# Kernel tuning notes

Measured on AMD Instinct MI355X. Metric: run time of the kernel, lower is better.

## Reference

```python
import jax, jax.numpy as jnp
import numpy as np

N = 50000
E = 800000
F_IN, F_HID, F_OUT = 128, 128, 64


def setup_inputs() -> dict:
    key = jax.random.key(0)
    ks = jax.random.split(key, 8)
    x = jax.random.normal(ks[0], (N, F_IN), dtype=jnp.float32)
    attn_edge_index = jax.random.randint(ks[1], (2, E), 0, N, dtype=jnp.int64)
    attn_edge_weight = jax.random.uniform(ks[2], (E,), dtype=jnp.float32)
    # GCNConv params (glorot-ish scale); PyG lin has no bias, conv bias added after aggregation
    W1 = jax.random.normal(ks[3], (F_IN, F_HID), dtype=jnp.float32) * (1.0 / np.sqrt(F_IN))
    b1 = jnp.zeros((F_HID,), dtype=jnp.float32)
    W2 = jax.random.normal(ks[4], (F_HID, F_OUT), dtype=jnp.float32) * (1.0 / np.sqrt(F_HID))
    b2 = jnp.zeros((F_OUT,), dtype=jnp.float32)
    return {"x": x, "attn_edge_index": attn_edge_index, "attn_edge_weight": attn_edge_weight,
            "W1": W1, "b1": b1, "W2": W2, "b2": b2}


def _gcn_norm(edge_index, edge_weight, num_nodes):
    # Add self-loops with weight 1 (PyG gcn_norm default)
    loop = jnp.arange(num_nodes, dtype=edge_index.dtype)
    src = jnp.concatenate([edge_index[0], loop])
    dst = jnp.concatenate([edge_index[1], loop])
    w = jnp.concatenate([edge_weight, jnp.ones((num_nodes,), edge_weight.dtype)])
    deg = jax.ops.segment_sum(w, dst, num_segments=num_nodes)  # in-degree weighted
    dinv = jnp.where(deg > 0, jax.lax.rsqrt(deg), 0.0)
    norm = dinv[src] * w * dinv[dst]  # symmetric normalization
    return src, dst, norm


def _gcn_conv(h, src, dst, norm, W, b, num_nodes):
    h = h @ W                                   # [N, Fout] dense transform
    msg = norm[:, None] * h[src]                # [E+N, Fout] gather-multiply
    out = jax.ops.segment_sum(msg, dst, num_segments=num_nodes)  # scatter-add
    return out + b


def reference(x, attn_edge_index, attn_edge_weight, W1, b1, W2, b2):
    num_nodes = x.shape[0]
    src, dst, norm = _gcn_norm(attn_edge_index, attn_edge_weight, num_nodes)
    h = _gcn_conv(x, src, dst, norm, W1, b1, num_nodes)
    h = jax.nn.relu(h)
    # dropout(p=0.5) is identity in eval mode
    h = _gcn_conv(h, src, dst, norm, W2, b2, num_nodes)
    return h
```

## Files before the change

### kernel.cpp

```cpp
#include <hip/hip_runtime.h>
#include <hip/hip_bf16.h>

static constexpr int FIN   = 128;
static constexpr int FHID  = 128;
static constexpr int FOUTC = 64;
static constexpr int CAP   = 64;

typedef short bf16x8 __attribute__((ext_vector_type(8)));
typedef float f32x4 __attribute__((ext_vector_type(4)));
typedef unsigned u32x4 __attribute__((ext_vector_type(4)));

__device__ __forceinline__ float bfbits2f(unsigned short u) {
  union { unsigned i; float f; } c; c.i = ((unsigned)u) << 16; return c.f;
}
__device__ __forceinline__ void unpack_bf2(unsigned u, float& lo, float& hi) {
  union { unsigned i; float f; } a, b;
  a.i = u << 16;
  b.i = u & 0xffff0000u;
  lo = a.f; hi = b.f;
}
__device__ __forceinline__ unsigned short f2bfbits(float f) {
  union { float fv; unsigned i; } c; c.fv = f;
  unsigned i = c.i;
  unsigned r = i + 0x7FFFu + ((i >> 16) & 1u);
  if ((i & 0x7F800000u) == 0x7F800000u) r = i;
  return (unsigned short)(r >> 16);
}
__device__ __forceinline__ int ld_idx(const void* ei, int is64, long long off) {
  return is64 ? (int)((const long long*)ei)[off] : ((const int*)ei)[off];
}
__device__ __forceinline__ float ld_f(const void* p, int isbf, long long i) {
  return isbf ? bfbits2f(((const unsigned short*)p)[i]) : ((const float*)p)[i];
}

__global__ void setup_kernel(const unsigned short* __restrict__ xb,
                             const unsigned* __restrict__ eiw,
                             const void* __restrict__ W1, const void* __restrict__ W2,
                             int* __restrict__ flags, unsigned short* __restrict__ Wt1,
                             unsigned short* __restrict__ Wt2, uint4* __restrict__ zr,
                             int nz4, int nztot) {
  const int tid = threadIdx.x;
  const int gid = blockIdx.x * 256 + tid;
  __shared__ int sflags[2];
  if (tid < 64) {
    unsigned short xs = xb[2 * tid];
    unsigned long long mb = __ballot(((xs >> 7) & 0xFFu) >= 0xC0u);
    unsigned long long m2 = __ballot(eiw[2 * tid + 1] != 0u);
    if (tid == 0) {
      sflags[0] = (mb == 0ull);
      sflags[1] = (m2 == 0ull);
      if (blockIdx.x == 0) { flags[0] = sflags[0]; flags[1] = sflags[1]; }
    }
  }
  __syncthreads();
  int f = sflags[0];
  if (blockIdx.x < 96) {
    int i = gid;
    if (i < 128 * 128) {
      int k = i >> 7, nn = i & 127;
      Wt1[nn * 128 + k] = f2bfbits(ld_f(W1, f, i));
    } else {
      int j = i - 128 * 128;
      int k = j >> 6, nn = j & 63;
      Wt2[nn * 128 + k] = f2bfbits(ld_f(W2, f, j));
    }
  }
  uint4 z = make_uint4(0u, 0u, 0u, 0u);
  for (int j = gid; j < nz4; j += gridDim.x * 256) zr[j] = z;
  if (gid == 0) {
    for (int j = nz4 * 4; j < nztot; ++j) ((unsigned*)zr)[j] = 0u;
  }
}

__global__ void fill_edges(const void* __restrict__ ei, const void* __restrict__ ew,
                           const int* __restrict__ flg, unsigned* __restrict__ cnt,
                           float* __restrict__ deg, unsigned* __restrict__ cedge, int E) {
  int g = blockIdx.x * 256 + threadIdx.x;
  if (g >= E) return;
  int is64 = flg[1], isbf = flg[0];
  int s = ld_idx(ei, is64, g);
  int d = ld_idx(ei, is64, (long long)E + g);
  float w = ld_f(ew, isbf, g);
  unsigned pos = atomicAdd(&cnt[d], 1u);
  atomicAdd(&deg[d], w);
  if (pos < (unsigned)CAP)
    cedge[(size_t)d * CAP + pos] = (((unsigned)s) << 16) | (unsigned)f2bfbits(w);
}

__launch_bounds__(256)
__global__ void gather_l1(const void* __restrict__ x, const int* __restrict__ flg,
                          const unsigned* __restrict__ cedge, const unsigned* __restrict__ cnt,
                          const float* __restrict__ deg, unsigned* __restrict__ agg, int n) {
  int wid = (blockIdx.x * 256 + threadIdx.x) >> 6;
  int lane = threadIdx.x & 63;
  if (wid >= n) return;
  unsigned e = __builtin_nontemporal_load(cedge + (size_t)wid * CAP + lane);
  int c = (int)cnt[wid];
  c = c > CAP ? CAP : c;
  float dw = deg[wid];
  float di = rsqrtf(1.f + dw);
  int rs = (lane < c) ? (int)(e >> 16) : wid;
  float ds = deg[rs];
  float wv = (lane < c) ? bfbits2f((unsigned short)(e & 0xFFFFu)) : 1.f;
  int cp = c + 1; if (cp > 64) cp = 64;
  float rw = (lane < cp) ? wv * rsqrtf(1.f + ds) : 0.f;
  int iters = (cp + 15) >> 4;

  if (flg[0]) {
    const uint4* xv = (const uint4*)x;
    const int fgrp = lane & 15, egrp = lane >> 4;
    float acc[8];
#pragma unroll
    for (int k = 0; k < 8; ++k) acc[k] = 0.f;

#define L1_LOAD(UA, UB, UC, UD, WA, WB, WC, WD, base)                       \
    {                                                                       \
      int i0 = (base) + egrp, i1 = i0 + 4, i2 = i0 + 8, i3 = i0 + 12;       \
      int s0 = __shfl(rs, i0), s1 = __shfl(rs, i1);                         \
      int s2 = __shfl(rs, i2), s3 = __shfl(rs, i3);                         \
      UA = xv[(size_t)s0 * 16 + fgrp];                                      \
      UB = xv[(size_t)s1 * 16 + fgrp];                                      \
      UC = xv[(size_t)s2 * 16 + fgrp];                                      \
      UD = xv[(size_t)s3 * 16 + fgrp];                                      \
      WA = __shfl(rw, i0); WB = __shfl(rw, i1);                             \
      WC = __shfl(rw, i2); WD = __shfl(rw, i3);                             \
    }
#define L1_FMA(U, W)                                                        \
    { float l, h;                                                           \
      unpack_bf2(U.x, l, h); acc[0]=fmaf(W,l,acc[0]); acc[1]=fmaf(W,h,acc[1]); \
      unpack_bf2(U.y, l, h); acc[2]=fmaf(W,l,acc[2]); acc[3]=fmaf(W,h,acc[3]); \
      unpack_bf2(U.z, l, h); acc[4]=fmaf(W,l,acc[4]); acc[5]=fmaf(W,h,acc[5]); \
      unpack_bf2(U.w, l, h); acc[6]=fmaf(W,l,acc[6]); acc[7]=fmaf(W,h,acc[7]); }
#define L1_FMA4(UA,UB,UC,UD,WA,WB,WC,WD) \
    L1_FMA(UA,WA) L1_FMA(UB,WB) L1_FMA(UC,WC) L1_FMA(UD,WD)

    uint4 a0, a1, a2, a3, b0, b1, b2, b3;
    float wa0, wa1, wa2, wa3, wb0, wb1, wb2, wb3;
    L1_LOAD(a0, a1, a2, a3, wa0, wa1, wa2, wa3, 0);
    if (iters > 1) {
      L1_LOAD(b0, b1, b2, b3, wb0, wb1, wb2, wb3, 16);
      L1_FMA4(a0, a1, a2, a3, wa0, wa1, wa2, wa3);
      if (iters > 2) {
        L1_LOAD(a0, a1, a2, a3, wa0, wa1, wa2, wa3, 32);
        L1_FMA4(b0, b1, b2, b3, wb0, wb1, wb2, wb3);
        if (iters > 3) {
          L1_LOAD(b0, b1, b2, b3, wb0, wb1, wb2, wb3, 48);
          L1_FMA4(a0, a1, a2, a3, wa0, wa1, wa2, wa3);
          L1_FMA4(b0, b1, b2, b3, wb0, wb1, wb2, wb3);
        } else {
          L1_FMA4(a0, a1, a2, a3, wa0, wa1, wa2, wa3);
        }
      } else {
        L1_FMA4(b0, b1, b2, b3, wb0, wb1, wb2, wb3);
      }
    } else {
      L1_FMA4(a0, a1, a2, a3, wa0, wa1, wa2, wa3);
    }
#undef L1_LOAD
#undef L1_FMA
#undef L1_FMA4

#pragma unroll
    for (int k = 0; k < 8; ++k) {
      acc[k] += __shfl_xor(acc[k], 16);
      acc[k] += __shfl_xor(acc[k], 32);
    }
    if (lane < 16) {
      float o0 = di * acc[0], o1 = di * acc[1], o2 = di * acc[2], o3 = di * acc[3];
      float o4 = di * acc[4], o5 = di * acc[5], o6 = di * acc[6], o7 = di * acc[7];
      u32x4 pk;
      pk.x = (unsigned)f2bfbits(o0) | ((unsigned)f2bfbits(o1) << 16);
      pk.y = (unsigned)f2bfbits(o2) | ((unsigned)f2bfbits(o3) << 16);
      pk.z = (unsigned)f2bfbits(o4) | ((unsigned)f2bfbits(o5) << 16);
      pk.w = (unsigned)f2bfbits(o6) | ((unsigned)f2bfbits(o7) << 16);
      __builtin_nontemporal_store(pk, (u32x4*)agg + (size_t)wid * 16 + fgrp);
    }
  } else {
    const float4* xf = (const float4*)x;
    const int fgrp = lane & 31, egrp = lane >> 5;
    float acc[4] = {0.f, 0.f, 0.f, 0.f};
    int it8 = (cp + 7) >> 3;
    for (int it = 0; it < it8; ++it) {
      int b = it * 8 + egrp;
#pragma unroll
      for (int t = 0; t < 4; ++t) {
        int idx = b + t * 2;
        int s = __shfl(rs, idx);
        float w = __shfl(rw, idx);
        float4 v = xf[(size_t)s * 32 + fgrp];
        acc[0] = fmaf(w, v.x, acc[0]); acc[1] = fmaf(w, v.y, acc[1]);
        acc[2] = fmaf(w, v.z, acc[2]); acc[3] = fmaf(w, v.w, acc[3]);
      }
    }
#pragma unroll
    for (int k = 0; k < 4; ++k) acc[k] += __shfl_xor(acc[k], 32);
    if (lane < 32) {
      float o0 = di * acc[0], o1 = di * acc[1], o2 = di * acc[2], o3 = di * acc[3];
      uint2 pk;
      pk.x = (unsigned)f2bfbits(o0) | ((unsigned)f2bfbits(o1) << 16);
      pk.y = (unsigned)f2bfbits(o2) | ((unsigned)f2bfbits(o3) << 16);
      ((uint2*)agg)[(size_t)wid * 32 + fgrp] = pk;
    }
  }
}

__launch_bounds__(256)
__global__ void gather_l2(const unsigned short* __restrict__ hw2, const int* __restrict__ flg,
                          const unsigned* __restrict__ cedge, const unsigned* __restrict__ cnt,
                          const float* __restrict__ deg, const void* __restrict__ b2,
                          void* __restrict__ out, int n) {
  int wid = (blockIdx.x * 256 + threadIdx.x) >> 6;
  int lane = threadIdx.x & 63;
  if (wid >= n) return;
  unsigned e = __builtin_nontemporal_load(cedge + (size_t)wid * CAP + lane);
  int c = (int)cnt[wid];
  c = c > CAP ? CAP : c;
  float dw = deg[wid];
  float di = rsqrtf(1.f + dw);
  int rs = (lane < c) ? (int)(e >> 16) : wid;
  float ds = deg[rs];
  float wv = (lane < c) ? bfbits2f((unsigned short)(e & 0xFFFFu)) : 1.f;
  int cp = c + 1; if (cp > 64) cp = 64;
  float rw = (lane < cp) ? wv * rsqrtf(1.f + ds) : 0.f;
  int iters = (cp + 15) >> 4;

  const uint4* hv = (const uint4*)hw2;
  const int fgrp = lane & 7, egrp = lane >> 3;
  float acc[8];
#pragma unroll
  for (int k = 0; k < 8; ++k) acc[k] = 0.f;

#define L2_LOAD(UA, UB, WA, WB, base)                                   \
  { int i0 = (base) + egrp, i1 = i0 + 8;                                \
    int s0 = __shfl(rs, i0), s1 = __shfl(rs, i1);                       \
    UA = hv[(size_t)s0 * 8 + fgrp];                                     \
    UB = hv[(size_t)s1 * 8 + fgrp];                                     \
    WA = __shfl(rw, i0); WB = __shfl(rw, i1); }
#define L2_FMA(U, W)                                                    \
  { float l, h;                                                         \
    unpack_bf2(U.x, l, h); acc[0]=fmaf(W,l,acc[0]); acc[1]=fmaf(W,h,acc[1]); \
    unpack_bf2(U.y, l, h); acc[2]=fmaf(W,l,acc[2]); acc[3]=fmaf(W,h,acc[3]); \
    unpack_bf2(U.z, l, h); acc[4]=fmaf(W,l,acc[4]); acc[5]=fmaf(W,h,acc[5]); \
    unpack_bf2(U.w, l, h); acc[6]=fmaf(W,l,acc[6]); acc[7]=fmaf(W,h,acc[7]); }
#define L2_FMA2(UA, UB, WA, WB) L2_FMA(UA, WA) L2_FMA(UB, WB)

  uint4 a0, a1, b0, b1;
  float wa0, wa1, wb0, wb1;
  L2_LOAD(a0, a1, wa0, wa1, 0);
  if (iters > 1) {
    L2_LOAD(b0, b1, wb0, wb1, 16);
    L2_FMA2(a0, a1, wa0, wa1);
    if (iters > 2) {
      L2_LOAD(a0, a1, wa0, wa1, 32);
      L2_FMA2(b0, b1, wb0, wb1);
      if (iters > 3) {
        L2_LOAD(b0, b1, wb0, wb1, 48);
        L2_FMA2(a0, a1, wa0, wa1);
        L2_FMA2(b0, b1, wb0, wb1);
      } else {
        L2_FMA2(a0, a1, wa0, wa1);
      }
    } else {
      L2_FMA2(b0, b1, wb0, wb1);
    }
  } else {
    L2_FMA2(a0, a1, wa0, wa1);
  }
#undef L2_LOAD
#undef L2_FMA
#undef L2_FMA2

#pragma unroll
  for (int k = 0; k < 8; ++k) {
    acc[k] += __shfl_xor(acc[k], 8);
    acc[k] += __shfl_xor(acc[k], 16);
    acc[k] += __shfl_xor(acc[k], 32);
  }
  if (lane < 8) {
    int isbf = flg[0];
    float o0 = di * acc[0] + ld_f(b2, isbf, fgrp * 8 + 0);
    float o1 = di * acc[1] + ld_f(b2, isbf, fgrp * 8 + 1);
    float o2 = di * acc[2] + ld_f(b2, isbf, fgrp * 8 + 2);
    float o3 = di * acc[3] + ld_f(b2, isbf, fgrp * 8 + 3);
    float o4 = di * acc[4] + ld_f(b2, isbf, fgrp * 8 + 4);
    float o5 = di * acc[5] + ld_f(b2, isbf, fgrp * 8 + 5);
    float o6 = di * acc[6] + ld_f(b2, isbf, fgrp * 8 + 6);
    float o7 = di * acc[7] + ld_f(b2, isbf, fgrp * 8 + 7);
    if (isbf) {
      uint4 pk;
      pk.x = (unsigned)f2bfbits(o0) | ((unsigned)f2bfbits(o1) << 16);
      pk.y = (unsigned)f2bfbits(o2) | ((unsigned)f2bfbits(o3) << 16);
      pk.z = (unsigned)f2bfbits(o4) | ((unsigned)f2bfbits(o5) << 16);
      pk.w = (unsigned)f2bfbits(o6) | ((unsigned)f2bfbits(o7) << 16);
      ((uint4*)out)[(size_t)wid * 8 + fgrp] = pk;
    } else {
      ((float4*)out)[(size_t)wid * 16 + fgrp * 2 + 0] = make_float4(o0, o1, o2, o3);
      ((float4*)out)[(size_t)wid * 16 + fgrp * 2 + 1] = make_float4(o4, o5, o6, o7);
    }
  }
}

__launch_bounds__(256)
__global__ void gemm12(const unsigned short* __restrict__ agg1,
                       const unsigned short* __restrict__ Wt1,
                       const unsigned short* __restrict__ Wt2,
                       const void* __restrict__ b1, const int* __restrict__ flg,
                       unsigned short* __restrict__ hw2, int M) {
  __shared__ unsigned short As[128 * 128];
  __shared__ unsigned short W1s[128 * 128];
  __shared__ unsigned short W2s[64 * 128];
  const int tid = threadIdx.x;
  const int r0 = blockIdx.x * 128;

  for (int i = tid; i < 128 * 16; i += 256) {
    int r = i >> 4, ch = i & 15;
    uint4 v = make_uint4(0u, 0u, 0u, 0u);
    if (r0 + r < M) v = *(const uint4*)(agg1 + (size_t)(r0 + r) * 128 + ch * 8);
    *(uint4*)&As[r * 128 + ((ch ^ (r & 15)) << 3)] = v;
  }
  for (int i = tid; i < 128 * 16; i += 256) {
    int r = i >> 4, ch = i & 15;
    uint4 v = *(const uint4*)(Wt1 + (size_t)r * 128 + ch * 8);
    *(uint4*)&W1s[r * 128 + ((ch ^ (r & 15)) << 3)] = v;
  }
  for (int i = tid; i < 64 * 16; i += 256) {
    int r = i >> 4, ch = i & 15;
    uint4 v = *(const uint4*)(Wt2 + (size_t)r * 128 + ch * 8);
    *(uint4*)&W2s[r * 128 + ((ch ^ (r & 15)) << 3)] = v;
  }
  __syncthreads();

  const int lane = tid & 63;
  const int wv = tid >> 6;
  const int ln15 = lane & 15;
  const int kq = lane >> 4;
  const int wbf = flg[0];

  f32x4 acc1[2][8];
#pragma unroll
  for (int mi = 0; mi < 2; ++mi)
#pragma unroll
    for (int nt = 0; nt < 8; ++nt) acc1[mi][nt] = (f32x4){0.f, 0.f, 0.f, 0.f};
#pragma unroll
  for (int kc = 0; kc < 4; ++kc) {
    int coff = (((kc * 4 + kq) ^ ln15) << 3);
    bf16x8 a0 = *(const bf16x8*)&As[((2 * wv + 0) * 16 + ln15) * 128 + coff];
    bf16x8 a1 = *(const bf16x8*)&As[((2 * wv + 1) * 16 + ln15) * 128 + coff];
#pragma unroll
    for (int nt = 0; nt < 8; ++nt) {
      bf16x8 b = *(const bf16x8*)&W1s[(nt * 16 + ln15) * 128 + coff];
      acc1[0][nt] = __builtin_amdgcn_mfma_f32_16x16x32_bf16(a0, b, acc1[0][nt], 0, 0, 0);
      acc1[1][nt] = __builtin_amdgcn_mfma_f32_16x16x32_bf16(a1, b, acc1[1][nt], 0, 0, 0);
    }
  }

#pragma unroll
  for (int nt = 0; nt < 8; ++nt) {
    int col = nt * 16 + ln15;
    float bv = ld_f(b1, wbf, col);
#pragma unroll
    for (int mi = 0; mi < 2; ++mi) {
#pragma unroll
      for (int r = 0; r < 4; ++r) {
        int row = 32 * wv + mi * 16 + kq * 4 + r;
        float o = fmaxf(acc1[mi][nt][r] + bv, 0.f);
        As[row * 128 + ((((col >> 3)) ^ (row & 15)) << 3) + (col & 7)] = f2bfbits(o);
      }
    }
  }
  __syncthreads();

  f32x4 acc2[2][4];
#pragma unroll
  for (int mi = 0; mi < 2; ++mi)
#pragma unroll
    for (int nt = 0; nt < 4; ++nt) acc2[mi][nt] = (f32x4){0.f, 0.f, 0.f, 0.f};
#pragma unroll
  for (int kc = 0; kc < 4; ++kc) {
    int coff = (((kc * 4 + kq) ^ ln15) << 3);
    bf16x8 a0 = *(const bf16x8*)&As[((2 * wv + 0) * 16 + ln15) * 128 + coff];
    bf16x8 a1 = *(const bf16x8*)&As[((2 * wv + 1) * 16 + ln15) * 128 + coff];
#pragma unroll
    for (int nt = 0; nt < 4; ++nt) {
      bf16x8 b = *(const bf16x8*)&W2s[(nt * 16 + ln15) * 128 + coff];
      acc2[0][nt] = __builtin_amdgcn_mfma_f32_16x16x32_bf16(a0, b, acc2[0][nt], 0, 0, 0);
      acc2[1][nt] = __builtin_amdgcn_mfma_f32_16x16x32_bf16(a1, b, acc2[1][nt], 0, 0, 0);
    }
  }
#pragma unroll
  for (int nt = 0; nt < 4; ++nt) {
    int col = nt * 16 + ln15;
#pragma unroll
    for (int mi = 0; mi < 2; ++mi) {
#pragma unroll
      for (int r = 0; r < 4; ++r) {
        int gr = r0 + 32 * wv + mi * 16 + kq * 4 + r;
        if (gr < M) hw2[(size_t)gr * 64 + col] = f2bfbits(acc2[mi][nt][r]);
      }
    }
  }
}

extern "C" void kernel_launch(void* const* d_in, const int* in_sizes, int n_in, void* d_out,
                              int out_size, void* d_ws, size_t ws_size, hipStream_t stream) {
  const void* x  = d_in[0];
  const void* ei = d_in[1];
  const void* ew = d_in[2];
  const void* W1 = d_in[3];
  const void* b1 = d_in[4];
  const void* W2 = d_in[5];
  const void* b2 = d_in[6];

  const int N = in_sizes[0] / FIN;
  const int E = in_sizes[1] / 2;
  const int B = 256;

  int* flags   = (int*)d_ws;
  unsigned* cnt = (unsigned*)(flags + 16);
  float* deg   = (float*)(cnt + N);
  unsigned short* Wt1 = (unsigned short*)(deg + N);
  unsigned short* Wt2 = Wt1 + 128 * 128;
  unsigned* cedge = (unsigned*)(Wt2 + 64 * 128);
  unsigned short* agg1 = (unsigned short*)(cedge + (size_t)N * CAP);
  unsigned short* hw2  = agg1 + (size_t)N * FHID;

  const int nztot = 2 * N;
  const int nz4 = nztot >> 2;

  setup_kernel<<<256, B, 0, stream>>>((const unsigned short*)x, (const unsigned*)ei, W1, W2,
                                      flags, Wt1, Wt2, (uint4*)cnt, nz4, nztot);
  fill_edges<<<(E + B - 1) / B, B, 0, stream>>>(ei, ew, flags, cnt, deg, cedge, E);
  gather_l1<<<(N + 3) / 4, B, 0, stream>>>(x, flags, cedge, cnt, deg, (unsigned*)agg1, N);
  gemm12<<<(N + 127) / 128, B, 0, stream>>>(agg1, Wt1, Wt2, b1, flags, hw2, N);
  gather_l2<<<(N + 3) / 4, B, 0, stream>>>(hw2, flags, cedge, cnt, deg, b2, d_out, N);
}
```

Baseline: 262.6 us.

## Build ELL adjacency with hashed CAS slots and compute degree in compaction pass

```diff
diff --git a/kernel.cpp b/kernel.cpp
--- a/kernel.cpp
+++ b/kernel.cpp
@@ -8,10 +8,17 @@
 
 typedef short bf16x8 __attribute__((ext_vector_type(8)));
 typedef float f32x4 __attribute__((ext_vector_type(4)));
+typedef unsigned u32x2 __attribute__((ext_vector_type(2)));
 typedef unsigned u32x4 __attribute__((ext_vector_type(4)));
 
 __device__ __forceinline__ float bfbits2f(unsigned short u) {
   union { unsigned i; float f; } c; c.i = ((unsigned)u) << 16; return c.f;
+}
+__device__ __forceinline__ float wbits2f(unsigned u) {
+  union { unsigned i; float f; } c; c.i = u; return c.f;
+}
+__device__ __forceinline__ unsigned f2wbits(float f) {
+  union { float fv; unsigned i; } c; c.fv = f; return c.i;
 }
 __device__ __forceinline__ void unpack_bf2(unsigned u, float& lo, float& hi) {
   union { unsigned i; float f; } a, b;
@@ -37,8 +44,8 @@
                              const unsigned* __restrict__ eiw,
                              const void* __restrict__ W1, const void* __restrict__ W2,
                              int* __restrict__ flags, unsigned short* __restrict__ Wt1,
-                             unsigned short* __restrict__ Wt2, uint4* __restrict__ zr,
-                             int nz4, int nztot) {
+                             unsigned short* __restrict__ Wt2, uint4* __restrict__ ellz,
+                             int nell4) {
   const int tid = threadIdx.x;
   const int gid = blockIdx.x * 256 + tid;
   __shared__ int sflags[2];
@@ -66,44 +73,83 @@
     }
   }
   uint4 z = make_uint4(0u, 0u, 0u, 0u);
-  for (int j = gid; j < nz4; j += gridDim.x * 256) zr[j] = z;
-  if (gid == 0) {
-    for (int j = nz4 * 4; j < nztot; ++j) ((unsigned*)zr)[j] = 0u;
-  }
-}
-
-__global__ void fill_edges(const void* __restrict__ ei, const void* __restrict__ ew,
-                           const int* __restrict__ flg, unsigned* __restrict__ cnt,
-                           float* __restrict__ deg, unsigned* __restrict__ cedge, int E) {
+  for (int j = gid; j < nell4; j += gridDim.x * 256) ellz[j] = z;
+}
+
+__global__ void fill_ell(const void* __restrict__ ei, const void* __restrict__ ew,
+                         const int* __restrict__ flg, unsigned long long* __restrict__ ell,
+                         int E, int half) {
   int g = blockIdx.x * 256 + threadIdx.x;
-  if (g >= E) return;
+  if (g >= half) return;
   int is64 = flg[1], isbf = flg[0];
-  int s = ld_idx(ei, is64, g);
-  int d = ld_idx(ei, is64, (long long)E + g);
-  float w = ld_f(ew, isbf, g);
-  unsigned pos = atomicAdd(&cnt[d], 1u);
-  atomicAdd(&deg[d], w);
-  if (pos < (unsigned)CAP)
-    cedge[(size_t)d * CAP + pos] = (((unsigned)s) << 16) | (unsigned)f2bfbits(w);
-}
-
-__launch_bounds__(256)
-__global__ void gather_l1(const void* __restrict__ x, const int* __restrict__ flg,
-                          const unsigned* __restrict__ cedge, const unsigned* __restrict__ cnt,
-                          const float* __restrict__ deg, unsigned* __restrict__ agg, int n) {
+  int sA = ld_idx(ei, is64, g);
+  int dA = ld_idx(ei, is64, (long long)E + g);
+  unsigned wA = f2wbits(ld_f(ew, isbf, g));
+  int eB = g + half;
+  bool hasB = eB < E;
+  int sB = 0, dB = 0;
+  unsigned wB = 0u;
+  if (hasB) {
+    sB = ld_idx(ei, is64, eB);
+    dB = ld_idx(ei, is64, (long long)E + eB);
+    wB = f2wbits(ld_f(ew, isbf, eB));
+  }
+  unsigned long long vA = ((unsigned long long)wA << 32) | (unsigned)sA;
+  unsigned long long vB = ((unsigned long long)wB << 32) | (unsigned)sB;
+  unsigned long long* rowA = ell + (size_t)dA * CAP;
+  unsigned long long* rowB = ell + (size_t)dB * CAP;
+  int pA = g & (CAP - 1), pB = eB & (CAP - 1);
+  bool doneA = (vA == 0ull);
+  bool doneB = !hasB || (vB == 0ull);
+  unsigned long long oA = doneA ? 0ull : atomicCAS(&rowA[pA], 0ull, vA);
+  unsigned long long oB = doneB ? 0ull : atomicCAS(&rowB[pB], 0ull, vB);
+  for (int t = 1; t < CAP && !doneA && oA != 0ull; ++t) {
+    pA = (pA + 1) & (CAP - 1);
+    oA = atomicCAS(&rowA[pA], 0ull, vA);
+  }
+  for (int t = 1; t < CAP && !doneB && oB != 0ull; ++t) {
+    pB = (pB + 1) & (CAP - 1);
+    oB = atomicCAS(&rowB[pB], 0ull, vB);
+  }
+}
+
+__global__ void dinv_compact(uint2* __restrict__ ell, float* __restrict__ dinv,
+                             unsigned* __restrict__ cedge, int n) {
   int wid = (blockIdx.x * 256 + threadIdx.x) >> 6;
   int lane = threadIdx.x & 63;
   if (wid >= n) return;
-  unsigned e = __builtin_nontemporal_load(cedge + (size_t)wid * CAP + lane);
-  int c = (int)cnt[wid];
-  c = c > CAP ? CAP : c;
-  float dw = deg[wid];
-  float di = rsqrtf(1.f + dw);
+  u32x2 rv = __builtin_nontemporal_load((const u32x2*)(ell + (size_t)wid * CAP) + lane);
+  float w = wbits2f(rv.y);
+  float ws = w;
+#pragma unroll
+  for (int off = 1; off < 64; off <<= 1) ws += __shfl_xor(ws, off);
+  bool valid = rv.y != 0u;
+  unsigned long long m = __ballot(valid);
+  int c = __popcll(m);
+  int rank = __popcll(m & ((1ull << lane) - 1ull));
+  int destl = valid ? rank : c + (lane - rank);
+  unsigned entry = valid ? ((rv.x << 16) | (unsigned)f2bfbits(w)) : 0u;
+  int pe = __builtin_amdgcn_ds_permute(destl << 2, (int)entry);
+  cedge[(size_t)wid * (CAP * 2) + lane] = (unsigned)pe;
+  if (lane == 0) dinv[wid] = rsqrtf(1.f + ws);
+}
+
+__launch_bounds__(256)
+__global__ void gather_l1(const void* __restrict__ x, const int* __restrict__ flg,
+                          const unsigned* __restrict__ cedge, const float* __restrict__ dinv,
+                          unsigned* __restrict__ agg, int n) {
+  int wid = (blockIdx.x * 256 + threadIdx.x) >> 6;
+  int lane = threadIdx.x & 63;
+  if (wid >= n) return;
+  unsigned e = __builtin_nontemporal_load(cedge + (size_t)wid * (CAP * 2) + lane);
+  unsigned long long m = __ballot(e != 0u);
+  int c = __popcll(m);
+  float di = dinv[wid];
   int rs = (lane < c) ? (int)(e >> 16) : wid;
-  float ds = deg[rs];
+  float dsrc = dinv[rs];
   float wv = (lane < c) ? bfbits2f((unsigned short)(e & 0xFFFFu)) : 1.f;
   int cp = c + 1; if (cp > 64) cp = 64;
-  float rw = (lane < cp) ? wv * rsqrtf(1.f + ds) : 0.f;
+  float rw = (lane < cp) ? wv * dsrc : 0.f;
   int iters = (cp + 15) >> 4;
 
   if (flg[0]) {
@@ -206,22 +252,20 @@
 
 __launch_bounds__(256)
 __global__ void gather_l2(const unsigned short* __restrict__ hw2, const int* __restrict__ flg,
-                          const unsigned* __restrict__ cedge, const unsigned* __restrict__ cnt,
-                          const float* __restrict__ deg, const void* __restrict__ b2,
-                          void* __restrict__ out, int n) {
+                          const unsigned* __restrict__ cedge, const float* __restrict__ dinv,
+                          const void* __restrict__ b2, void* __restrict__ out, int n) {
   int wid = (blockIdx.x * 256 + threadIdx.x) >> 6;
   int lane = threadIdx.x & 63;
   if (wid >= n) return;
-  unsigned e = __builtin_nontemporal_load(cedge + (size_t)wid * CAP + lane);
-  int c = (int)cnt[wid];
-  c = c > CAP ? CAP : c;
-  float dw = deg[wid];
-  float di = rsqrtf(1.f + dw);
+  unsigned e = __builtin_nontemporal_load(cedge + (size_t)wid * (CAP * 2) + lane);
+  unsigned long long m = __ballot(e != 0u);
+  int c = __popcll(m);
+  float di = dinv[wid];
   int rs = (lane < c) ? (int)(e >> 16) : wid;
-  float ds = deg[rs];
+  float dsrc = dinv[rs];
   float wv = (lane < c) ? bfbits2f((unsigned short)(e & 0xFFFFu)) : 1.f;
   int cp = c + 1; if (cp > 64) cp = 64;
-  float rw = (lane < cp) ? wv * rsqrtf(1.f + ds) : 0.f;
+  float rw = (lane < cp) ? wv * dsrc : 0.f;
   int iters = (cp + 15) >> 4;
 
   const uint4* hv = (const uint4*)hw2;
@@ -416,21 +460,20 @@
   const int B = 256;
 
   int* flags   = (int*)d_ws;
-  unsigned* cnt = (unsigned*)(flags + 16);
-  float* deg   = (float*)(cnt + N);
-  unsigned short* Wt1 = (unsigned short*)(deg + N);
+  float* dinv  = (float*)(flags + 16);
+  unsigned short* Wt1 = (unsigned short*)(dinv + N);
   unsigned short* Wt2 = Wt1 + 128 * 128;
-  unsigned* cedge = (unsigned*)(Wt2 + 64 * 128);
-  unsigned short* agg1 = (unsigned short*)(cedge + (size_t)N * CAP);
+  unsigned long long* ell = (unsigned long long*)(Wt2 + 64 * 128);
+  unsigned* cedge = (unsigned*)ell;
+  unsigned short* agg1 = (unsigned short*)(ell + (size_t)N * CAP);
   unsigned short* hw2  = agg1 + (size_t)N * FHID;
 
-  const int nztot = 2 * N;
-  const int nz4 = nztot >> 2;
-
-  setup_kernel<<<256, B, 0, stream>>>((const unsigned short*)x, (const unsigned*)ei, W1, W2,
-                                      flags, Wt1, Wt2, (uint4*)cnt, nz4, nztot);
-  fill_edges<<<(E + B - 1) / B, B, 0, stream>>>(ei, ew, flags, cnt, deg, cedge, E);
-  gather_l1<<<(N + 3) / 4, B, 0, stream>>>(x, flags, cedge, cnt, deg, (unsigned*)agg1, N);
+  const int half = (E + 1) / 2;
+  setup_kernel<<<512, B, 0, stream>>>((const unsigned short*)x, (const unsigned*)ei, W1, W2,
+                                      flags, Wt1, Wt2, (uint4*)ell, N * CAP / 2);
+  fill_ell<<<(half + B - 1) / B, B, 0, stream>>>(ei, ew, flags, ell, E, half);
+  dinv_compact<<<(N + 3) / 4, B, 0, stream>>>((uint2*)ell, dinv, cedge, N);
+  gather_l1<<<(N + 3) / 4, B, 0, stream>>>(x, flags, cedge, dinv, (unsigned*)agg1, N);
   gemm12<<<(N + 127) / 128, B, 0, stream>>>(agg1, Wt1, Wt2, b1, flags, hw2, N);
-  gather_l2<<<(N + 3) / 4, B, 0, stream>>>(hw2, flags, cedge, cnt, deg, b2, d_out, N);
-}
+  gather_l2<<<(N + 3) / 4, B, 0, stream>>>(hw2, flags, cedge, dinv, b2, d_out, N);
+}
```

Measured after the change: 231.3 us (median of 2 runs). -11.9%, faster.
